# Optimization experiments

Hardware: AMD Instinct MI355X
Metric: run time of the kernel (lower is better)

Reference implementation:

```python
import jax, jax.numpy as jnp
import numpy as np

V, E, H, T, C, B, S = 50000, 256, 512, 50, 5, 128, 512
FC1 = 500


def setup_inputs() -> dict:
    key = jax.random.key(0)
    ks = jax.random.split(key, 13)
    n = lambda i, shape, sc: (jax.random.normal(ks[i], shape, jnp.float32) * sc)
    return {
        "x": jax.random.randint(ks[0], (B, S), 0, V),
        "topic": n(1, (B, T), 1.0),
        "h0": n(2, (B, H), 1.0),
        "c0": n(3, (B, H), 1.0),
        "embed": n(4, (V, E), 0.05),
        "W_x": n(5, (E, 4 * H), 0.02),
        "W_t": n(6, (T, 4 * H), 0.02),
        "W_h": n(7, (H, 4 * H), 0.02),
        "b": jnp.zeros((4 * H,), jnp.float32),
        "fc1_w": n(8, (FC1, H), 0.02),
        "fc1_b": jnp.zeros((FC1,), jnp.float32),
        "fc2_w": n(9, (C, FC1), 0.02),
        "fc2_b": jnp.zeros((C,), jnp.float32),
    }


def reference(x, topic, h0, c0, embed, W_x, W_t, W_h, b, fc1_w, fc1_b, fc2_w, fc2_b):
    # Embedding lookup: [B,S,E] -> time-major [S,B,E]
    x_emb = jnp.transpose(embed[x], (1, 0, 2))
    # Precompute input + topic gate contributions (topic is constant per step)
    gx = jnp.einsum("sbe,eg->sbg", x_emb, W_x) + (topic @ W_t + b)[None]  # [S,B,4H]

    def step(carry, g):
        h, c = carry
        g = g + h @ W_h
        i, f, gg, o = jnp.split(g, 4, axis=-1)
        i = jax.nn.sigmoid(i)
        f = jax.nn.sigmoid(f)
        gg = jnp.tanh(gg)
        o = jax.nn.sigmoid(o)
        c = f * c + i * gg
        h = o * jnp.tanh(c)
        return (h, c), None

    (h_last, _), _ = jax.lax.scan(step, (h0, c0), gx)
    # MLP head (dropout = identity in eval)
    hid = h_last @ fc1_w.T + fc1_b
    logits = hid @ fc2_w.T + fc2_b
    return logits
```

## Files before the change

kernel.cpp:

```cpp
#include <hip/hip_runtime.h>
#include <hip/hip_bf16.h>

typedef unsigned short u16;
typedef unsigned int u32;
typedef __attribute__((ext_vector_type(8))) short short8;
typedef __attribute__((ext_vector_type(4))) float f32x4;


__device__ __forceinline__ float bf2f(u16 v){ union{u32 u; float f;} x; x.u = ((u32)v)<<16; return x.f; }
__device__ __forceinline__ u16 f2bf(float f){ union{float f; u32 u;} x; x.f = f; u32 r = ((x.u>>16)&1u) + 0x7FFFu; return (u16)((x.u + r)>>16); }
__device__ __forceinline__ float sigf(float x){ return 1.f/(1.f+__expf(-x)); }
__device__ __forceinline__ float tanh_f(float x){ return 2.f/(1.f+__expf(-2.f*x)) - 1.f; }

#define POLL_GUARD (1u<<20)

__global__ void k_prep(const float* __restrict__ Wh, const float* __restrict__ Wx,
                       u16* __restrict__ WhT, u16* __restrict__ WxT){
  __shared__ u16 tile[32][33];
  int b = blockIdx.x;
  const float* src; u16* dst; int K, kt, nt;
  if (b < 1024){ src = Wh; dst = WhT; K = 512; kt = b & 15; nt = b >> 4; }
  else { b -= 1024; src = Wx; dst = WxT; K = 256; kt = b & 7; nt = b >> 3; }
  int tx = threadIdx.x, ty = threadIdx.y;
  #pragma unroll
  for (int p = 0; p < 4; ++p){
    int r = p*8 + ty;
    tile[r][tx] = f2bf(src[(kt*32 + r)*2048 + nt*32 + tx]);
  }
  __syncthreads();
  #pragma unroll
  for (int p = 0; p < 4; ++p){
    int r = p*8 + ty;
    dst[(nt*32 + r)*K + kt*32 + tx] = tile[tx][r];
  }
}

__global__ void k_topic(const float* __restrict__ topic, const float* __restrict__ Wt,
                        const float* __restrict__ bias, float* __restrict__ tb){
  int b = blockIdx.y;
  int col = blockIdx.x*256 + threadIdx.x;
  float acc = bias[col];
  #pragma unroll 5
  for (int t = 0; t < 50; ++t)
    acc += topic[b*50 + t] * Wt[t*2048 + col];
  tb[b*2048 + col] = acc;
}

__global__ void k_init(const float* __restrict__ h0, u16* __restrict__ hhi,
                       u16* __restrict__ hlo, u32* __restrict__ cnt){
  if (blockIdx.x < 256){
    int i = blockIdx.x*256 + threadIdx.x;
    float v = h0[i];
    u16 hi = f2bf(v);
    hhi[i] = hi;
    hlo[i] = f2bf(v - bf2f(hi));
  } else {
    cnt[threadIdx.x] = 0;
  }
}

__global__ void __launch_bounds__(256, 1)
k_rnn(const int* __restrict__ x, const float* __restrict__ embed, const float* __restrict__ c0,
      const u16* __restrict__ WhT, const u16* __restrict__ WxT, const float* __restrict__ tb,
      u16* __restrict__ hhi, u16* __restrict__ hlo, float* __restrict__ hf, u32* cnt)
{
  const int bx = blockIdx.x;
  const int g = bx & 15;
  const int w = bx >> 4;
  const int tid = threadIdx.x;
  const int v = tid >> 6;
  const int lane = tid & 63;
  const int l15 = lane & 15, l4 = lane >> 4;
  const int arr = l15 & 7;
  const int pl  = l15 >> 3;

  __shared__ __align__(16) u16 ldsH[2][8][512];
  __shared__ __align__(16) float ldsD[16][132];
  __shared__ int ldsX[8][512];

  const int er = tid >> 5, ehc = tid & 31;
  const int eb = g*8 + er;
  const int ecol = w*32 + ehc;
  float c_val = c0[eb*512 + ecol];
  const float tb0 = tb[eb*2048 +    0 + ecol];
  const float tb1 = tb[eb*2048 +  512 + ecol];
  const float tb2 = tb[eb*2048 + 1024 + ecol];
  const float tb3 = tb[eb*2048 + 1536 + ecol];

  short8 b2[2][16], b1[2][8];
  #pragma unroll
  for (int j = 0; j < 2; ++j){
    const int cl = (2*v + j)*16 + l15;
    const int cg = (cl & 3)*512 + w*32 + (cl >> 2);
    #pragma unroll
    for (int kt = 0; kt < 16; ++kt)
      b2[j][kt] = *(const short8*)(WhT + cg*512 + kt*32 + l4*8);
    #pragma unroll
    for (int kt = 0; kt < 8; ++kt)
      b1[j][kt] = *(const short8*)(WxT + cg*256 + kt*32 + l4*8);
  }

  {
    const int4* src = (const int4*)(x + g*4096);
    int4* dst = (int4*)&ldsX[0][0];
    #pragma unroll
    for (int i = 0; i < 4; ++i) dst[tid + 256*i] = src[tid + 256*i];
  }
  __syncthreads();

  const short8 z8 = {0,0,0,0,0,0,0,0};
  short8 a1A[8], a1B[8];
  {
    const int idx0 = ldsX[arr][0];
    const float* ep = embed + (u32)idx0*256 + l4*8;
    #pragma unroll
    for (int kt = 0; kt < 8; ++kt){
      float4 f0 = *(const float4*)(ep + kt*32);
      float4 f1 = *(const float4*)(ep + kt*32 + 4);
      union { short8 s; u32 u[4]; } pk;
      asm("v_cvt_pk_bf16_f32 %0, %1, %2" : "=v"(pk.u[0]) : "v"(f0.x), "v"(f0.y));
      asm("v_cvt_pk_bf16_f32 %0, %1, %2" : "=v"(pk.u[1]) : "v"(f0.z), "v"(f0.w));
      asm("v_cvt_pk_bf16_f32 %0, %1, %2" : "=v"(pk.u[2]) : "v"(f1.x), "v"(f1.y));
      asm("v_cvt_pk_bf16_f32 %0, %1, %2" : "=v"(pk.u[3]) : "v"(f1.z), "v"(f1.w));
      a1A[kt] = (l15 < 8) ? pk.s : z8;
    }
  }

  const int sr = tid >> 5;
  const int j31 = tid & 31;
  const int ph0 = (2*j31) ^ (((2*j31) >> 3) ^ sr);
  const int ph1 = ph0 ^ 1;

  auto step = [&](int t, short8 (&a1c)[8], short8 (&a1n)[8]){
    const int tn = (t < 511) ? t + 1 : 511;
    const int idxn = ldsX[arr][tn];
    const float* ep = embed + (u32)idxn*256 + l4*8;
    f32x4 e[16];
    #pragma unroll
    for (int kt = 0; kt < 8; ++kt){
      asm volatile("global_load_dwordx4 %0, %2, off\n\t"
                   "global_load_dwordx4 %1, %3, off"
                   : "=v"(e[2*kt]), "=v"(e[2*kt+1])
                   : "v"(ep + kt*32), "v"(ep + kt*32 + 4));
    }
    f32x4 aX0 = {0.f,0.f,0.f,0.f}, aX1 = {0.f,0.f,0.f,0.f};
    #pragma unroll
    for (int kt = 0; kt < 8; ++kt){
      aX0 = __builtin_amdgcn_mfma_f32_16x16x32_bf16(a1c[kt], b1[0][kt], aX0, 0, 0, 0);
      aX1 = __builtin_amdgcn_mfma_f32_16x16x32_bf16(a1c[kt], b1[1][kt], aX1, 0, 0, 0);
    }
    if (t > 0){
      const u32 tgt = (u32)t;
      const u32* fp = cnt + (g*16 + (lane & 15));
      bool ok; u32 guard = 0;
      do {
        u32 cv;
        asm volatile("global_load_dword %0, %1, off sc0 sc1\n\ts_waitcnt vmcnt(0)"
                     : "=v"(cv) : "v"(fp) : "memory");
        ok = __all((int)(lane >= 16 || cv >= tgt)) != 0;
      } while (!ok && ++guard < POLL_GUARD);
    }
    {
      const u16* sh = hhi + (t & 1)*65536 + g*4096 + tid*16;
      const u16* sl = hlo + (t & 1)*65536 + g*4096 + tid*16;
      f32x4 h0, h1, q0, q1;
      asm volatile("global_load_dwordx4 %0, %2, off sc0 sc1\n\t"
                   "global_load_dwordx4 %1, %3, off sc0 sc1"
                   : "=v"(h0), "=v"(h1) : "v"(sh), "v"(sh + 8));
      asm volatile("global_load_dwordx4 %0, %2, off sc0 sc1\n\t"
                   "global_load_dwordx4 %1, %3, off sc0 sc1"
                   : "=v"(q0), "=v"(q1) : "v"(sl), "v"(sl + 8));
      asm volatile("s_waitcnt vmcnt(0)" ::: "memory");
      asm volatile("" : "+v"(h0), "+v"(h1), "+v"(q0), "+v"(q1));
      *(f32x4*)&ldsH[0][sr][ph0*8] = h0;
      *(f32x4*)&ldsH[0][sr][ph1*8] = h1;
      *(f32x4*)&ldsH[1][sr][ph0*8] = q0;
      *(f32x4*)&ldsH[1][sr][ph1*8] = q1;
    }
    __syncthreads();
    f32x4 c0a = {0.f,0.f,0.f,0.f}, c0b = {0.f,0.f,0.f,0.f};
    f32x4 c1a = {0.f,0.f,0.f,0.f}, c1b = {0.f,0.f,0.f,0.f};
    #pragma unroll
    for (int kt = 0; kt < 8; ++kt){
      const int gg = kt*4 + l4;
      const int ph = gg ^ ((gg >> 3) ^ arr);
      short8 ah = *(const short8*)&ldsH[pl][arr][ph*8];
      c0a = __builtin_amdgcn_mfma_f32_16x16x32_bf16(ah, b2[0][kt], c0a, 0, 0, 0);
      c1a = __builtin_amdgcn_mfma_f32_16x16x32_bf16(ah, b2[1][kt], c1a, 0, 0, 0);
    }
    #pragma unroll
    for (int kt = 8; kt < 16; ++kt){
      const int gg = kt*4 + l4;
      const int ph = gg ^ ((gg >> 3) ^ arr);
      short8 ah = *(const short8*)&ldsH[pl][arr][ph*8];
      c0b = __builtin_amdgcn_mfma_f32_16x16x32_bf16(ah, b2[0][kt], c0b, 0, 0, 0);
      c1b = __builtin_amdgcn_mfma_f32_16x16x32_bf16(ah, b2[1][kt], c1b, 0, 0, 0);
    }
    const f32x4 acc0 = (aX0 + c0a) + c0b;
    const f32x4 acc1 = (aX1 + c1a) + c1b;
    #pragma unroll
    for (int jj = 0; jj < 4; ++jj){
      ldsD[l4*4 + jj][(2*v + 0)*16 + l15] = acc0[jj];
      ldsD[l4*4 + jj][(2*v + 1)*16 + l15] = acc1[jj];
    }
    __syncthreads();
    const f32x4 pa = *(const f32x4*)&ldsD[er][ehc*4];
    const f32x4 pb = *(const f32x4*)&ldsD[er + 8][ehc*4];
    const float iv = sigf(pa[0] + pb[0] + tb0);
    const float fv = sigf(pa[1] + pb[1] + tb1);
    const float gv = tanh_f(pa[2] + pb[2] + tb2);
    const float ov = sigf(pa[3] + pb[3] + tb3);
    c_val = fv*c_val + iv*gv;
    const float hval = ov*tanh_f(c_val);
    if (t < 511){
      const u16 hi = f2bf(hval);
      const u16 lo = f2bf(hval - bf2f(hi));
      const int np_ = (t + 1) & 1;
      u16* dh = hhi + np_*65536 + eb*512 + ecol;
      u16* dl = hlo + np_*65536 + eb*512 + ecol;
      asm volatile("global_store_short %0, %1, off sc0 sc1" :: "v"(dh), "v"((u32)hi) : "memory");
      asm volatile("global_store_short %0, %1, off sc0 sc1" :: "v"(dl), "v"((u32)lo) : "memory");
    } else {
      hf[eb*512 + ecol] = hval;
    }
    asm volatile("s_waitcnt vmcnt(0)" ::: "memory");
    __syncthreads();
    if (tid == 0 && t < 511){
      const u32 fv_ = (u32)(t + 1);
      u32* fp = cnt + (g*16 + w);
      asm volatile("global_store_dword %0, %1, off sc0 sc1" :: "v"(fp), "v"(fv_) : "memory");
    }
    #pragma unroll
    for (int kt = 0; kt < 8; ++kt){
      union { short8 s; u32 u[4]; } pk;
      asm volatile("v_cvt_pk_bf16_f32 %0, %1, %2" : "=v"(pk.u[0]) : "v"(e[2*kt][0]),   "v"(e[2*kt][1]));
      asm volatile("v_cvt_pk_bf16_f32 %0, %1, %2" : "=v"(pk.u[1]) : "v"(e[2*kt][2]),   "v"(e[2*kt][3]));
      asm volatile("v_cvt_pk_bf16_f32 %0, %1, %2" : "=v"(pk.u[2]) : "v"(e[2*kt+1][0]), "v"(e[2*kt+1][1]));
      asm volatile("v_cvt_pk_bf16_f32 %0, %1, %2" : "=v"(pk.u[3]) : "v"(e[2*kt+1][2]), "v"(e[2*kt+1][3]));
      a1n[kt] = (l15 < 8) ? pk.s : z8;
    }
  };

  for (int t = 0; t < 512; t += 2){
    step(t,     a1A, a1B);
    step(t + 1, a1B, a1A);
  }
}

__global__ void k_head1(const float* __restrict__ hf, const float* __restrict__ w1,
                        const float* __restrict__ b1v, float* __restrict__ hid){
  int b = blockIdx.y;
  int j = blockIdx.x*256 + threadIdx.x;
  if (j >= 500) return;
  float acc = b1v[j];
  const float* hr = hf + b*512;
  const float* wr = w1 + j*512;
  for (int k = 0; k < 512; ++k) acc += hr[k]*wr[k];
  hid[b*500 + j] = acc;
}

__global__ void k_head2(const float* __restrict__ hid, const float* __restrict__ w2,
                        const float* __restrict__ b2v, float* __restrict__ out){
  int o = blockIdx.x*256 + threadIdx.x;
  if (o >= 640) return;
  int b = o / 5, cls = o % 5;
  float acc = b2v[cls];
  const float* hr = hid + b*500;
  const float* wr = w2 + cls*500;
  for (int j = 0; j < 500; ++j) acc += hr[j]*wr[j];
  out[o] = acc;
}

extern "C" void kernel_launch(void* const* d_in, const int* in_sizes, int n_in,
                              void* d_out, int out_size, void* d_ws, size_t ws_size,
                              hipStream_t stream) {
  const int*   x     = (const int*)d_in[0];
  const float* topic = (const float*)d_in[1];
  const float* h0    = (const float*)d_in[2];
  const float* c0    = (const float*)d_in[3];
  const float* embed = (const float*)d_in[4];
  const float* Wx    = (const float*)d_in[5];
  const float* Wt    = (const float*)d_in[6];
  const float* Wh    = (const float*)d_in[7];
  const float* bias  = (const float*)d_in[8];
  const float* fc1w  = (const float*)d_in[9];
  const float* fc1b  = (const float*)d_in[10];
  const float* fc2w  = (const float*)d_in[11];
  const float* fc2b  = (const float*)d_in[12];

  char* ws = (char*)d_ws;
  u16*   WhT = (u16*)(ws + 0);
  u16*   WxT = (u16*)(ws + 2097152);
  float* tb  = (float*)(ws + 3145728);
  u16*   hhi = (u16*)(ws + 4194304);
  u16*   hlo = (u16*)(ws + 4456448);
  float* hf  = (float*)(ws + 4718592);
  float* hid = (float*)(ws + 4980736);
  u32*   cnt = (u32*)(ws + 5236736);

  k_prep<<<dim3(1536), dim3(32, 8), 0, stream>>>(Wh, Wx, WhT, WxT);
  k_topic<<<dim3(8, 128), dim3(256), 0, stream>>>(topic, Wt, bias, tb);
  k_init<<<dim3(257), dim3(256), 0, stream>>>(h0, hhi, hlo, cnt);

  k_rnn<<<dim3(256), dim3(256), 0, stream>>>(x, embed, c0, WhT, WxT, tb, hhi, hlo, hf, cnt);

  k_head1<<<dim3(2, 128), dim3(256), 0, stream>>>(hf, fc1w, fc1b, hid);
  k_head2<<<dim3(3), dim3(256), 0, stream>>>(hid, fc2w, fc2b, (float*)d_out);
}
```

Before: 2.088 ms.

## Embed step counters in 16-byte h packets to replace separate flag polling

Replaces the per-workgroup counter flags with packed 16-byte packets that carry six bf16 hidden values plus the step number in one dword. Consumers poll the packets themselves, so one poll both synchronises and delivers the data. This removes the separate flag round-trip and the trailing barrier plus flag store on the producer side. It costs more polling traffic (six 16-byte loads per thread per retry), an LDS repack stage, a padded LDS layout, and a smaller poll guard that could let a slow producer be skipped silently.

```diff
diff --git a/kernel.cpp b/kernel.cpp
--- a/kernel.cpp
+++ b/kernel.cpp
@@ -12,7 +12,8 @@
 __device__ __forceinline__ float sigf(float x){ return 1.f/(1.f+__expf(-x)); }
 __device__ __forceinline__ float tanh_f(float x){ return 2.f/(1.f+__expf(-2.f*x)) - 1.f; }
 
-#define POLL_GUARD (1u<<20)
+#define POLL_GUARD (1u<<14)
+
 
 __global__ void k_prep(const float* __restrict__ Wh, const float* __restrict__ Wx,
                        u16* __restrict__ WhT, u16* __restrict__ WxT){
@@ -46,23 +47,39 @@
   tb[b*2048 + col] = acc;
 }
 
-__global__ void k_init(const float* __restrict__ h0, u16* __restrict__ hhi,
-                       u16* __restrict__ hlo, u32* __restrict__ cnt){
-  if (blockIdx.x < 256){
-    int i = blockIdx.x*256 + threadIdx.x;
-    float v = h0[i];
-    u16 hi = f2bf(v);
-    hhi[i] = hi;
-    hlo[i] = f2bf(v - bf2f(hi));
+__global__ void k_init(const float* __restrict__ h0, u32* __restrict__ U){
+  int uid = blockIdx.x*256 + threadIdx.x;
+  int parity = (uid >= 24576) ? 1 : 0;
+  int rem = uid - parity*24576;
+  int g     = rem / 1536;   int r2 = rem - g*1536;
+  int plane = r2 / 768;     int pid = r2 - plane*768;
+  int row   = pid / 96;     int p3 = pid - row*96;
+  int prod  = p3 / 6;       int u  = p3 - prod*6;
+  u32 d0=0, d1=0, d2=0, d3;
+  if (parity == 0){
+    const float* hr = h0 + (g*8 + row)*512 + prod*32 + u*6;
+    int nv = 32 - u*6; if (nv > 6) nv = 6;
+    u16 vals[6] = {0,0,0,0,0,0};
+    for (int j = 0; j < nv; ++j){
+      float v = hr[j];
+      u16 hi = f2bf(v);
+      vals[j] = plane ? f2bf(v - bf2f(hi)) : hi;
+    }
+    d0 = (u32)vals[0] | ((u32)vals[1]<<16);
+    d1 = (u32)vals[2] | ((u32)vals[3]<<16);
+    d2 = (u32)vals[4] | ((u32)vals[5]<<16);
+    d3 = 0u;
   } else {
-    cnt[threadIdx.x] = 0;
-  }
+    d3 = 0xFFFFFFFFu;
+  }
+  u32* dst = U + (size_t)uid*4;
+  dst[0]=d0; dst[1]=d1; dst[2]=d2; dst[3]=d3;
 }
 
 __global__ void __launch_bounds__(256, 1)
 k_rnn(const int* __restrict__ x, const float* __restrict__ embed, const float* __restrict__ c0,
       const u16* __restrict__ WhT, const u16* __restrict__ WxT, const float* __restrict__ tb,
-      u16* __restrict__ hhi, u16* __restrict__ hlo, float* __restrict__ hf, u32* cnt)
+      u32* __restrict__ U, float* __restrict__ hf)
 {
   const int bx = blockIdx.x;
   const int g = bx & 15;
@@ -74,9 +91,10 @@
   const int arr = l15 & 7;
   const int pl  = l15 >> 3;
 
-  __shared__ __align__(16) u16 ldsH[2][8][512];
+  __shared__ __align__(16) u16 ldsH[2][8][704];
   __shared__ __align__(16) float ldsD[16][132];
   __shared__ int ldsX[8][512];
+  __shared__ u32 ldsP[8][32];
 
   const int er = tid >> 5, ehc = tid & 31;
   const int eb = g*8 + er;
@@ -108,6 +126,29 @@
   }
   __syncthreads();
 
+  int rw0,rw1,rw2, cb0,cb1,cb2; u32 of0,of1,of2;
+  {
+    int pid, row, p3, prod, u;
+    pid = tid*3 + 0; row = pid/96; p3 = pid - row*96; prod = p3/6; u = p3 - prod*6;
+    rw0 = row; cb0 = prod*40 + u*6 + row*8; of0 = (u32)((((g*2+0)*8+row)*16+prod)*6+u);
+    pid = tid*3 + 1; row = pid/96; p3 = pid - row*96; prod = p3/6; u = p3 - prod*6;
+    rw1 = row; cb1 = prod*40 + u*6 + row*8; of1 = (u32)((((g*2+0)*8+row)*16+prod)*6+u);
+    pid = tid*3 + 2; row = pid/96; p3 = pid - row*96; prod = p3/6; u = p3 - prod*6;
+    rw2 = row; cb2 = prod*40 + u*6 + row*8; of2 = (u32)((((g*2+0)*8+row)*16+prod)*6+u);
+  }
+  int pk_plane=0, pk_row=0, pk_ucol=0, pk_nv=0; u32 pk_off=0;
+  if (tid < 96){
+    pk_plane = tid/48; int rem = tid - pk_plane*48;
+    pk_row = rem/6; int u = rem - pk_row*6;
+    pk_ucol = u*6;
+    pk_nv = 32 - pk_ucol; if (pk_nv > 6) pk_nv = 6;
+    pk_off = (u32)((((g*2+pk_plane)*8+pk_row)*16 + w)*6 + u);
+  }
+  int goff[16];
+  #pragma unroll
+  for (int kt = 0; kt < 16; ++kt) goff[kt] = kt*40 + l4*8 + arr*8;
+  const u16* hrow = &ldsH[pl][arr][0];
+
   const short8 z8 = {0,0,0,0,0,0,0,0};
   short8 a1A[8], a1B[8];
   {
@@ -126,10 +167,7 @@
     }
   }
 
-  const int sr = tid >> 5;
-  const int j31 = tid & 31;
-  const int ph0 = (2*j31) ^ (((2*j31) >> 3) ^ sr);
-  const int ph1 = ph0 ^ 1;
+  union F4 { f32x4 f; u32 u[4]; };
 
   auto step = [&](int t, short8 (&a1c)[8], short8 (&a1n)[8]){
     const int tn = (t < 511) ? t + 1 : 511;
@@ -149,50 +187,51 @@
       aX0 = __builtin_amdgcn_mfma_f32_16x16x32_bf16(a1c[kt], b1[0][kt], aX0, 0, 0, 0);
       aX1 = __builtin_amdgcn_mfma_f32_16x16x32_bf16(a1c[kt], b1[1][kt], aX1, 0, 0, 0);
     }
-    if (t > 0){
-      const u32 tgt = (u32)t;
-      const u32* fp = cnt + (g*16 + (lane & 15));
+    F4 H0,H1,H2,L0,L1,L2;
+    {
+      const u32* b = U + (size_t)((t & 1)*24576)*4;
+      const u32 *a0 = b + (size_t)of0*4,      *a1_ = b + (size_t)of1*4,      *a2 = b + (size_t)of2*4;
+      const u32 *a3 = b + (size_t)(of0+768)*4,*a4 = b + (size_t)(of1+768)*4, *a5 = b + (size_t)(of2+768)*4;
+      const u32 tg = (u32)t;
       bool ok; u32 guard = 0;
       do {
-        u32 cv;
-        asm volatile("global_load_dword %0, %1, off sc0 sc1\n\ts_waitcnt vmcnt(0)"
-                     : "=v"(cv) : "v"(fp) : "memory");
-        ok = __all((int)(lane >= 16 || cv >= tgt)) != 0;
+        asm volatile(
+          "global_load_dwordx4 %0, %6, off sc0 sc1\n\t"
+          "global_load_dwordx4 %1, %7, off sc0 sc1\n\t"
+          "global_load_dwordx4 %2, %8, off sc0 sc1\n\t"
+          "global_load_dwordx4 %3, %9, off sc0 sc1\n\t"
+          "global_load_dwordx4 %4, %10, off sc0 sc1\n\t"
+          "global_load_dwordx4 %5, %11, off sc0 sc1\n\t"
+          "s_waitcnt vmcnt(0)"
+          : "=&v"(H0.f), "=&v"(H1.f), "=&v"(H2.f), "=&v"(L0.f), "=&v"(L1.f), "=&v"(L2.f)
+          : "v"(a0), "v"(a1_), "v"(a2), "v"(a3), "v"(a4), "v"(a5)
+          : "memory");
+        int mine = (H0.u[3]==tg) && (H1.u[3]==tg) && (H2.u[3]==tg)
+                && (L0.u[3]==tg) && (L1.u[3]==tg) && (L2.u[3]==tg);
+        ok = __all(mine) != 0;
       } while (!ok && ++guard < POLL_GUARD);
     }
     {
-      const u16* sh = hhi + (t & 1)*65536 + g*4096 + tid*16;
-      const u16* sl = hlo + (t & 1)*65536 + g*4096 + tid*16;
-      f32x4 h0, h1, q0, q1;
-      asm volatile("global_load_dwordx4 %0, %2, off sc0 sc1\n\t"
-                   "global_load_dwordx4 %1, %3, off sc0 sc1"
-                   : "=v"(h0), "=v"(h1) : "v"(sh), "v"(sh + 8));
-      asm volatile("global_load_dwordx4 %0, %2, off sc0 sc1\n\t"
-                   "global_load_dwordx4 %1, %3, off sc0 sc1"
-                   : "=v"(q0), "=v"(q1) : "v"(sl), "v"(sl + 8));
-      asm volatile("s_waitcnt vmcnt(0)" ::: "memory");
-      asm volatile("" : "+v"(h0), "+v"(h1), "+v"(q0), "+v"(q1));
-      *(f32x4*)&ldsH[0][sr][ph0*8] = h0;
-      *(f32x4*)&ldsH[0][sr][ph1*8] = h1;
-      *(f32x4*)&ldsH[1][sr][ph0*8] = q0;
-      *(f32x4*)&ldsH[1][sr][ph1*8] = q1;
+      u16* p;
+      p = &ldsH[0][rw0][cb0]; *(u32*)p = H0.u[0]; *(u32*)(p+2) = H0.u[1]; *(u32*)(p+4) = H0.u[2];
+      p = &ldsH[0][rw1][cb1]; *(u32*)p = H1.u[0]; *(u32*)(p+2) = H1.u[1]; *(u32*)(p+4) = H1.u[2];
+      p = &ldsH[0][rw2][cb2]; *(u32*)p = H2.u[0]; *(u32*)(p+2) = H2.u[1]; *(u32*)(p+4) = H2.u[2];
+      p = &ldsH[1][rw0][cb0]; *(u32*)p = L0.u[0]; *(u32*)(p+2) = L0.u[1]; *(u32*)(p+4) = L0.u[2];
+      p = &ldsH[1][rw1][cb1]; *(u32*)p = L1.u[0]; *(u32*)(p+2) = L1.u[1]; *(u32*)(p+4) = L1.u[2];
+      p = &ldsH[1][rw2][cb2]; *(u32*)p = L2.u[0]; *(u32*)(p+2) = L2.u[1]; *(u32*)(p+4) = L2.u[2];
     }
     __syncthreads();
     f32x4 c0a = {0.f,0.f,0.f,0.f}, c0b = {0.f,0.f,0.f,0.f};
     f32x4 c1a = {0.f,0.f,0.f,0.f}, c1b = {0.f,0.f,0.f,0.f};
     #pragma unroll
     for (int kt = 0; kt < 8; ++kt){
-      const int gg = kt*4 + l4;
-      const int ph = gg ^ ((gg >> 3) ^ arr);
-      short8 ah = *(const short8*)&ldsH[pl][arr][ph*8];
+      short8 ah = *(const short8*)(hrow + goff[kt]);
       c0a = __builtin_amdgcn_mfma_f32_16x16x32_bf16(ah, b2[0][kt], c0a, 0, 0, 0);
       c1a = __builtin_amdgcn_mfma_f32_16x16x32_bf16(ah, b2[1][kt], c1a, 0, 0, 0);
     }
     #pragma unroll
     for (int kt = 8; kt < 16; ++kt){
-      const int gg = kt*4 + l4;
-      const int ph = gg ^ ((gg >> 3) ^ arr);
-      short8 ah = *(const short8*)&ldsH[pl][arr][ph*8];
+      short8 ah = *(const short8*)(hrow + goff[kt]);
       c0b = __builtin_amdgcn_mfma_f32_16x16x32_bf16(ah, b2[0][kt], c0b, 0, 0, 0);
       c1b = __builtin_amdgcn_mfma_f32_16x16x32_bf16(ah, b2[1][kt], c1b, 0, 0, 0);
     }
@@ -212,24 +251,33 @@
     const float ov = sigf(pa[3] + pb[3] + tb3);
     c_val = fv*c_val + iv*gv;
     const float hval = ov*tanh_f(c_val);
-    if (t < 511){
+    {
       const u16 hi = f2bf(hval);
       const u16 lo = f2bf(hval - bf2f(hi));
-      const int np_ = (t + 1) & 1;
-      u16* dh = hhi + np_*65536 + eb*512 + ecol;
-      u16* dl = hlo + np_*65536 + eb*512 + ecol;
-      asm volatile("global_store_short %0, %1, off sc0 sc1" :: "v"(dh), "v"((u32)hi) : "memory");
-      asm volatile("global_store_short %0, %1, off sc0 sc1" :: "v"(dl), "v"((u32)lo) : "memory");
-    } else {
-      hf[eb*512 + ecol] = hval;
+      ldsP[er][ehc] = (u32)hi | ((u32)lo << 16);
+    }
+    if (t == 511) hf[eb*512 + ecol] = hval;
+    __syncthreads();
+    if (t < 511 && tid < 96){
+      u32 x0 = ldsP[pk_row][(pk_ucol+0) & 31];
+      u32 x1 = ldsP[pk_row][(pk_ucol+1) & 31];
+      u32 x2 = ldsP[pk_row][(pk_ucol+2) & 31];
+      u32 x3 = ldsP[pk_row][(pk_ucol+3) & 31];
+      u32 x4 = ldsP[pk_row][(pk_ucol+4) & 31];
+      u32 x5 = ldsP[pk_row][(pk_ucol+5) & 31];
+      if (pk_nv < 6){ x2 = 0; x3 = 0; x4 = 0; x5 = 0; }
+      u16 v0,v1,v2,v3,v4,v5;
+      if (pk_plane){ v0=(u16)(x0>>16); v1=(u16)(x1>>16); v2=(u16)(x2>>16); v3=(u16)(x3>>16); v4=(u16)(x4>>16); v5=(u16)(x5>>16); }
+      else        { v0=(u16)x0; v1=(u16)x1; v2=(u16)x2; v3=(u16)x3; v4=(u16)x4; v5=(u16)x5; }
+      F4 D;
+      D.u[0] = (u32)v0 | ((u32)v1<<16);
+      D.u[1] = (u32)v2 | ((u32)v3<<16);
+      D.u[2] = (u32)v4 | ((u32)v5<<16);
+      D.u[3] = (u32)(t + 1);
+      u32* dst = U + (size_t)(((u32)((t+1)&1))*24576 + pk_off)*4;
+      asm volatile("global_store_dwordx4 %0, %1, off sc0 sc1" :: "v"(dst), "v"(D.f) : "memory");
     }
     asm volatile("s_waitcnt vmcnt(0)" ::: "memory");
-    __syncthreads();
-    if (tid == 0 && t < 511){
-      const u32 fv_ = (u32)(t + 1);
-      u32* fp = cnt + (g*16 + w);
-      asm volatile("global_store_dword %0, %1, off sc0 sc1" :: "v"(fp), "v"(fv_) : "memory");
-    }
     #pragma unroll
     for (int kt = 0; kt < 8; ++kt){
       union { short8 s; u32 u[4]; } pk;
@@ -292,17 +340,15 @@
   u16*   WhT = (u16*)(ws + 0);
   u16*   WxT = (u16*)(ws + 2097152);
   float* tb  = (float*)(ws + 3145728);
-  u16*   hhi = (u16*)(ws + 4194304);
-  u16*   hlo = (u16*)(ws + 4456448);
-  float* hf  = (float*)(ws + 4718592);
-  float* hid = (float*)(ws + 4980736);
-  u32*   cnt = (u32*)(ws + 5236736);
+  u32*   U   = (u32*)(ws + 4194304);
+  float* hf  = (float*)(ws + 4980736);
+  float* hid = (float*)(ws + 3145728);
 
   k_prep<<<dim3(1536), dim3(32, 8), 0, stream>>>(Wh, Wx, WhT, WxT);
   k_topic<<<dim3(8, 128), dim3(256), 0, stream>>>(topic, Wt, bias, tb);
-  k_init<<<dim3(257), dim3(256), 0, stream>>>(h0, hhi, hlo, cnt);
-
-  k_rnn<<<dim3(256), dim3(256), 0, stream>>>(x, embed, c0, WhT, WxT, tb, hhi, hlo, hf, cnt);
+  k_init<<<dim3(192), dim3(256), 0, stream>>>(h0, U);
+
+  k_rnn<<<dim3(256), dim3(256), 0, stream>>>(x, embed, c0, WhT, WxT, tb, U, hf);
 
   k_head1<<<dim3(2, 128), dim3(256), 0, stream>>>(hf, fc1w, fc1b, hid);
   k_head2<<<dim3(3), dim3(256), 0, stream>>>(hid, fc2w, fc2b, (float*)d_out);
```

Result: faster. 1.931 ms (-7.5%).
